# Performance work log

Measured on AMD Instinct MI355X. Metric: run time of the kernel, lower is better.

The kernel has to match this reference:

```python
import jax, jax.numpy as jnp
import numpy as np

N = 100000   # n_nodes
E = 1600000  # n_edges
BN_EPS = 1e-5


def setup_inputs() -> dict:
    key = jax.random.key(0)
    ks = jax.random.split(key, 10)
    x = jax.random.normal(ks[0], (N, 20), dtype=jnp.float32)
    edge_index = jax.random.randint(ks[1], (2, E), 0, N, dtype=jnp.int64)
    dims = [(20, 64), (64, 48), (48, 32)]
    inp = {"x": x, "edge_index": edge_index}
    for i, (di, do) in enumerate(dims):
        inp[f"W{i+1}"] = jax.random.normal(ks[2 + i], (di, do), dtype=jnp.float32) / np.sqrt(di)
        inp[f"b{i+1}"] = jnp.zeros((do,), dtype=jnp.float32)
        inp[f"g{i+1}"] = jnp.ones((do,), dtype=jnp.float32)
        inp[f"beta{i+1}"] = jnp.zeros((do,), dtype=jnp.float32)
    return inp


def _gcn_norm(edge_index):
    # add self loops, compute symmetric normalization D^-1/2 (A+I) D^-1/2
    loop = jnp.arange(N, dtype=edge_index.dtype)
    src = jnp.concatenate([edge_index[0], loop])
    dst = jnp.concatenate([edge_index[1], loop])
    deg = jax.ops.segment_sum(jnp.ones_like(src, dtype=jnp.float32), dst, num_segments=N)
    dinv = jax.lax.rsqrt(deg)  # deg >= 1 thanks to self loops
    norm = dinv[src] * dinv[dst]  # [E+N]
    return src, dst, norm


def _gcn_layer(h, src, dst, norm, W, b):
    m = h @ W                                  # [N, out]
    agg = jax.ops.segment_sum(m[src] * norm[:, None], dst, num_segments=N)
    return agg + b


def _batchnorm(x, g, beta):
    mu = jnp.mean(x, axis=0)
    var = jnp.mean(jnp.square(x - mu), axis=0)  # biased, as torch BN training
    return (x - mu) * jax.lax.rsqrt(var + BN_EPS) * g + beta


def reference(x, edge_index, W1, b1, g1, beta1, W2, b2, g2, beta2, W3, b3, g3, beta3):
    src, dst, norm = _gcn_norm(edge_index)
    h = _gcn_layer(x, src, dst, norm, W1, b1)
    h = jax.nn.relu(_batchnorm(h, g1, beta1))   # dropout rate 0 -> identity
    h = _gcn_layer(h, src, dst, norm, W2, b2)
    h = jax.nn.relu(_batchnorm(h, g2, beta2))
    h = _gcn_layer(h, src, dst, norm, W3, b3)
    h = _batchnorm(h, g3, beta3)                # last activation is Identity
    return h
```

## Files before the change

### kernel.cpp

```cpp
#include <hip/hip_runtime.h>


#define NN 100000
#define NE 1600000
constexpr float BN_EPS_F = 1e-5f;
constexpr float INVN = 1.f / (float)NN;

#define BSZ 128
#define NBKT ((NN + BSZ - 1) / BSZ)
#define EC 16384
#define NEB ((NE + EC - 1) / EC)
#define MTOT (NBKT * NEB)
#define CAP 4096


__device__ __forceinline__ unsigned f2bf(float f) {
  union { float f; unsigned u; } v; v.f = f;
  return (v.u + 0x7fffu + ((v.u >> 16) & 1u)) >> 16;
}
__device__ __forceinline__ unsigned pack_bf2(float f0, float f1) {
  return f2bf(f0) | (f2bf(f1) << 16);
}
__device__ __forceinline__ float bf_lo(unsigned u) {
  union { unsigned u; float f; } v; v.u = u << 16; return v.f;
}
__device__ __forceinline__ float bf_hi(unsigned u) {
  union { unsigned u; float f; } v; v.u = u & 0xffff0000u; return v.f;
}


__global__ void hist_pass(const int* __restrict__ dst, int* __restrict__ ph, int e) {
  __shared__ int h[NBKT];
  int tid = threadIdx.x;
  for (int i = tid; i < NBKT; i += 256) h[i] = 0;
  __syncthreads();
  int tbase = blockIdx.x * EC + tid * 64;
#pragma unroll 4
  for (int k = 0; k < 64; k += 4) {
    int i = tbase + k;
    if (i < e) {
      int4 d = *(const int4*)(dst + i);
      atomicAdd(&h[d.x >> 7], 1);
      atomicAdd(&h[d.y >> 7], 1);
      atomicAdd(&h[d.z >> 7], 1);
      atomicAdd(&h[d.w >> 7], 1);
    }
  }
  __syncthreads();
  for (int i = tid; i < NBKT; i += 256) ph[i * NEB + blockIdx.x] = h[i];
}

__global__ void scan_block_sums(const int* __restrict__ data, int* __restrict__ bsums, int n) {
  __shared__ int sd[256];
  int tid = threadIdx.x;
  int base = blockIdx.x * 1024;
  int s = 0;
#pragma unroll
  for (int j = 0; j < 4; j++) {
    int idx = base + tid * 4 + j;
    if (idx < n) s += data[idx];
  }
  sd[tid] = s;
  __syncthreads();
  for (int o = 128; o > 0; o >>= 1) {
    if (tid < o) sd[tid] += sd[tid + o];
    __syncthreads();
  }
  if (tid == 0) bsums[blockIdx.x] = sd[0];
}

__global__ void scan_bsums2(int* __restrict__ bsums, int nb) {
  __shared__ int sd[128];
  int tid = threadIdx.x;
  int v = (tid < nb) ? bsums[tid] : 0;
  sd[tid] = v;
  __syncthreads();
  for (int o = 1; o < 128; o <<= 1) {
    int t = (tid >= o) ? sd[tid - o] : 0;
    __syncthreads();
    sd[tid] += t;
    __syncthreads();
  }
  if (tid < nb) bsums[tid] = sd[tid] - v;
}

__global__ void scan_apply(int* __restrict__ data, const int* __restrict__ bsums, int n) {
  __shared__ int sd[256];
  int tid = threadIdx.x;
  int base = blockIdx.x * 1024;
  int c[4];
  int s = 0;
#pragma unroll
  for (int j = 0; j < 4; j++) {
    int idx = base + tid * 4 + j;
    c[j] = (idx < n) ? data[idx] : 0;
    s += c[j];
  }
  sd[tid] = s;
  __syncthreads();
  for (int o = 1; o < 256; o <<= 1) {
    int t = (tid >= o) ? sd[tid - o] : 0;
    __syncthreads();
    sd[tid] += t;
    __syncthreads();
  }
  int off = bsums[blockIdx.x] + sd[tid] - s;
#pragma unroll
  for (int j = 0; j < 4; j++) {
    int idx = base + tid * 4 + j;
    if (idx < n) {
      data[idx] = off;
      off += c[j];
    }
  }
}

__global__ void bin_pass(const int* __restrict__ src, const int* __restrict__ dst,
                         const int* __restrict__ ph, int* __restrict__ packed, int e) {
  __shared__ int cur[NBKT];
  int tid = threadIdx.x;
  for (int i = tid; i < NBKT; i += 256) cur[i] = ph[i * NEB + blockIdx.x];
  __syncthreads();
  int tbase = blockIdx.x * EC + tid * 64;
#pragma unroll 4
  for (int k = 0; k < 64; k += 4) {
    int i = tbase + k;
    if (i < e) {
      int4 s = *(const int4*)(src + i);
      int4 d = *(const int4*)(dst + i);
      int p0 = atomicAdd(&cur[d.x >> 7], 1);
      int p1 = atomicAdd(&cur[d.y >> 7], 1);
      int p2 = atomicAdd(&cur[d.z >> 7], 1);
      int p3 = atomicAdd(&cur[d.w >> 7], 1);
      packed[p0] = (s.x << 7) | (d.x & 127);
      packed[p1] = (s.y << 7) | (d.y & 127);
      packed[p2] = (s.z << 7) | (d.z & 127);
      packed[p3] = (s.w << 7) | (d.w & 127);
    }
  }
}

__global__ void bucket_finalize(const int* __restrict__ ph, const int* __restrict__ packed,
                                const float* __restrict__ x, int* __restrict__ rowptr,
                                float* __restrict__ dinv, int* __restrict__ csr_src,
                                unsigned* __restrict__ xb) {
  __shared__ int eidx[CAP];
  __shared__ int csr_l[CAP];
  __shared__ int ldeg[BSZ], lscan[BSZ], lcur[BSZ];
  __shared__ float ldinv[BSZ];
  int b = blockIdx.x, tid = threadIdx.x;
  int start = ph[b * NEB];
  int end = (b == NBKT - 1) ? NE : ph[(b + 1) * NEB];
  int cnt = end - start;
  if (cnt > CAP) cnt = CAP;
  for (int i = tid; i < cnt; i += 256) eidx[i] = packed[start + i];
  if (tid < BSZ) ldeg[tid] = 0;
  __syncthreads();
  for (int i = tid; i < cnt; i += 256) atomicAdd(&ldeg[eidx[i] & 127], 1);
  __syncthreads();
  if (tid < BSZ) lscan[tid] = ldeg[tid];
  __syncthreads();
  for (int o = 1; o < BSZ; o <<= 1) {
    int t = 0;
    if (tid < BSZ && tid >= o) t = lscan[tid - o];
    __syncthreads();
    if (tid < BSZ) lscan[tid] += t;
    __syncthreads();
  }
  int gn = b * BSZ + tid;
  if (tid < BSZ) {
    int ex = lscan[tid] - ldeg[tid];
    lcur[tid] = ex;
    float dv = rsqrtf((float)(ldeg[tid] + 1));
    ldinv[tid] = dv;
    if (gn < NN) {
      rowptr[gn] = start + ex;
      dinv[gn] = dv;
    }
  }
  if (b == NBKT - 1 && tid == 0) rowptr[NN] = NE;
  __syncthreads();
  for (int i = tid; i < cnt; i += 256) {
    int pe = eidx[i];
    int pos = atomicAdd(&lcur[pe & 127], 1);
    csr_l[pos] = pe >> 7;
  }
  __syncthreads();
  for (int i = tid; i < cnt; i += 256) csr_src[start + i] = csr_l[i];
  for (int i = tid; i < BSZ * 16; i += 256) {
    int nl = i >> 4, j = i & 15;
    int g2 = b * BSZ + nl;
    if (g2 < NN) {
      unsigned u = 0;
      if (j < 10) {
        float2 f = *(const float2*)(x + (size_t)g2 * 20 + 2 * j);
        float dd = ldinv[nl];
        u = pack_bf2(dd * f.x, dd * f.y);
      }
      xb[(size_t)g2 * 16 + j] = u;
    }
  }
}


__launch_bounds__(256)
__global__ void agg1_gemm1(const unsigned* __restrict__ mb, const int* __restrict__ rowptr,
                           const int* __restrict__ csr_src, const float* __restrict__ dinv,
                           const float* __restrict__ W1, const float* __restrict__ b1,
                           unsigned* __restrict__ h1u, float* __restrict__ gsum) {
  __shared__ float Wl[20 * 64];
  __shared__ float Hl[16][20];
  __shared__ float4 sbuf[256];
  int tid = threadIdx.x;
  for (int i = tid; i < 20 * 64; i += 256) Wl[i] = W1[i];
  int sub = tid >> 4, lane = tid & 15;
  int cl = (lane < 10) ? lane : lane - 10;
  int d = blockIdx.x * 16 + sub;
  int start = rowptr[d], end = rowptr[d + 1];
  unsigned su = mb[(size_t)d * 16 + cl];
  float acc0 = bf_lo(su), acc1 = bf_hi(su);
  int end1 = end - 1;
  for (int base = start; base < end; base += 16) {
    unsigned u[16];
#pragma unroll
    for (int t = 0; t < 16; t++) {
      int jt = base + t;
      int jc = jt < end1 ? jt : end1;
      unsigned uu = mb[(size_t)csr_src[jc] * 16 + cl];
      u[t] = (jt < end) ? uu : 0u;
    }
#pragma unroll
    for (int t = 0; t < 16; t++) { acc0 += bf_lo(u[t]); acc1 += bf_hi(u[t]); }
  }
  float dd = dinv[d];
  if (lane < 10) {
    Hl[sub][2 * cl] = dd * acc0;
    Hl[sub][2 * cl + 1] = dd * acc1;
  }
  __syncthreads();
  int cg = lane;
  float a0 = b1[4 * cg], a1 = b1[4 * cg + 1], a2 = b1[4 * cg + 2], a3 = b1[4 * cg + 3];
#pragma unroll
  for (int k = 0; k < 20; k++) {
    float a = Hl[sub][k];
    const float* w = &Wl[k * 64 + 4 * cg];
    a0 = fmaf(a, w[0], a0);
    a1 = fmaf(a, w[1], a1);
    a2 = fmaf(a, w[2], a2);
    a3 = fmaf(a, w[3], a3);
  }
  *(uint2*)(h1u + (size_t)d * 32 + 2 * cg) = make_uint2(pack_bf2(a0, a1), pack_bf2(a2, a3));
  sbuf[tid] = make_float4(a0, a1, a2, a3);
  __syncthreads();
  float* gs = gsum + (blockIdx.x & 7) * 128;
  if (tid < 16) {
    float s0 = 0.f, s1 = 0.f, s2 = 0.f, s3 = 0.f;
#pragma unroll
    for (int k = 0; k < 16; k++) {
      float4 a = sbuf[k * 16 + tid];
      s0 += a.x; s1 += a.y; s2 += a.z; s3 += a.w;
    }
    atomicAdd(&gs[4 * tid], s0);
    atomicAdd(&gs[4 * tid + 1], s1);
    atomicAdd(&gs[4 * tid + 2], s2);
    atomicAdd(&gs[4 * tid + 3], s3);
  }
  __syncthreads();
  sbuf[tid] = make_float4(a0 * a0, a1 * a1, a2 * a2, a3 * a3);
  __syncthreads();
  if (tid < 16) {
    float q0 = 0.f, q1 = 0.f, q2 = 0.f, q3 = 0.f;
#pragma unroll
    for (int k = 0; k < 16; k++) {
      float4 b = sbuf[k * 16 + tid];
      q0 += b.x; q1 += b.y; q2 += b.z; q3 += b.w;
    }
    atomicAdd(&gs[64 + 4 * tid], q0);
    atomicAdd(&gs[64 + 4 * tid + 1], q1);
    atomicAdd(&gs[64 + 4 * tid + 2], q2);
    atomicAdd(&gs[64 + 4 * tid + 3], q3);
  }
}


__launch_bounds__(256)
__global__ void gemm2_bf(const unsigned* __restrict__ hu, const float* __restrict__ W,
                         const float* __restrict__ gsum, const float* __restrict__ g,
                         const float* __restrict__ beta, const float* __restrict__ dinv,
                         unsigned* __restrict__ out) {
  __shared__ float Wl[64 * 48];
  __shared__ float Hl[16][64];
  __shared__ float scl[64], sft[64];
  int tid = threadIdx.x;
  int row0 = blockIdx.x * 16;
  if (tid < 64) {
    float s = 0.f, q = 0.f;
    for (int b = 0; b < 8; b++) {
      s += gsum[b * 128 + tid];
      q += gsum[b * 128 + 64 + tid];
    }
    float mean = s * INVN;
    float var = fmaxf(q * INVN - mean * mean, 0.f);
    float inv = rsqrtf(var + BN_EPS_F);
    float sc = g[tid] * inv;
    scl[tid] = sc;
    sft[tid] = beta[tid] - mean * sc;
  }
  for (int i = tid; i < 64 * 48; i += 256) Wl[i] = W[i];
  __syncthreads();
  for (int i = tid; i < 16 * 32; i += 256) {
    int r = i >> 5, j = i & 31;
    unsigned u = hu[(size_t)(row0 + r) * 32 + j];
    Hl[r][2 * j] = fmaxf(fmaf(bf_lo(u), scl[2 * j], sft[2 * j]), 0.f);
    Hl[r][2 * j + 1] = fmaxf(fmaf(bf_hi(u), scl[2 * j + 1], sft[2 * j + 1]), 0.f);
  }
  __syncthreads();
  int r = tid >> 4, c = tid & 15;
  if (c < 12) {
    float a0 = 0.f, a1 = 0.f, a2 = 0.f, a3 = 0.f;
#pragma unroll
    for (int k = 0; k < 64; k++) {
      float a = Hl[r][k];
      const float* w = &Wl[k * 48 + 4 * c];
      a0 = fmaf(a, w[0], a0);
      a1 = fmaf(a, w[1], a1);
      a2 = fmaf(a, w[2], a2);
      a3 = fmaf(a, w[3], a3);
    }
    float dd = dinv[row0 + r];
    uint2 uo = make_uint2(pack_bf2(dd * a0, dd * a1), pack_bf2(dd * a2, dd * a3));
    *(uint2*)(out + (size_t)(row0 + r) * 24 + 2 * c) = uo;
  }
}


__launch_bounds__(256)
__global__ void aggregate_bf48(const uint2* __restrict__ mb, const int* __restrict__ rowptr,
                               const int* __restrict__ csr_src, const float* __restrict__ dinv,
                               const float* __restrict__ bias, unsigned* __restrict__ out,
                               float* __restrict__ gsum) {
  __shared__ float4 sbuf[256];
  int tid = threadIdx.x;
  int sub = tid >> 4, lane = tid & 15;
  int cl = (lane < 12) ? lane : lane - 12;
  int d = blockIdx.x * 16 + sub;
  int start = rowptr[d], end = rowptr[d + 1];
  uint2 su = mb[(size_t)d * 12 + cl];
  float acc0 = bf_lo(su.x), acc1 = bf_hi(su.x), acc2 = bf_lo(su.y), acc3 = bf_hi(su.y);
  int end1 = end - 1;
  for (int base = start; base < end; base += 16) {
    uint2 u[16];
#pragma unroll
    for (int t = 0; t < 16; t++) {
      int jt = base + t;
      int jc = jt < end1 ? jt : end1;
      uint2 uu = mb[(size_t)csr_src[jc] * 12 + cl];
      u[t].x = (jt < end) ? uu.x : 0u;
      u[t].y = (jt < end) ? uu.y : 0u;
    }
#pragma unroll
    for (int t = 0; t < 16; t++) {
      acc0 += bf_lo(u[t].x); acc1 += bf_hi(u[t].x);
      acc2 += bf_lo(u[t].y); acc3 += bf_hi(u[t].y);
    }
  }
  float dd = dinv[d];
  float v0 = dd * acc0 + bias[4 * cl];
  float v1 = dd * acc1 + bias[4 * cl + 1];
  float v2 = dd * acc2 + bias[4 * cl + 2];
  float v3 = dd * acc3 + bias[4 * cl + 3];
  if (lane >= 12) { v0 = v1 = v2 = v3 = 0.f; }
  if (lane < 12) {
    uint2 uo = make_uint2(pack_bf2(v0, v1), pack_bf2(v2, v3));
    *(uint2*)(out + (size_t)d * 24 + 2 * cl) = uo;
  }
  sbuf[tid] = make_float4(v0, v1, v2, v3);
  __syncthreads();
  float* gs = gsum + (blockIdx.x & 7) * 128;
  if (tid < 12) {
    float s0 = 0.f, s1 = 0.f, s2 = 0.f, s3 = 0.f;
#pragma unroll
    for (int k = 0; k < 16; k++) {
      float4 a = sbuf[k * 16 + tid];
      s0 += a.x; s1 += a.y; s2 += a.z; s3 += a.w;
    }
    atomicAdd(&gs[4 * tid], s0);
    atomicAdd(&gs[4 * tid + 1], s1);
    atomicAdd(&gs[4 * tid + 2], s2);
    atomicAdd(&gs[4 * tid + 3], s3);
  }
  __syncthreads();
  sbuf[tid] = make_float4(v0 * v0, v1 * v1, v2 * v2, v3 * v3);
  __syncthreads();
  if (tid < 12) {
    float q0 = 0.f, q1 = 0.f, q2 = 0.f, q3 = 0.f;
#pragma unroll
    for (int k = 0; k < 16; k++) {
      float4 b = sbuf[k * 16 + tid];
      q0 += b.x; q1 += b.y; q2 += b.z; q3 += b.w;
    }
    atomicAdd(&gs[64 + 4 * tid], q0);
    atomicAdd(&gs[64 + 4 * tid + 1], q1);
    atomicAdd(&gs[64 + 4 * tid + 2], q2);
    atomicAdd(&gs[64 + 4 * tid + 3], q3);
  }
}


__launch_bounds__(256)
__global__ void gemm3_bf(const unsigned* __restrict__ hu, const float* __restrict__ W,
                         const float* __restrict__ gsum, const float* __restrict__ g,
                         const float* __restrict__ beta, const float* __restrict__ dinv,
                         unsigned* __restrict__ out) {
  __shared__ float Wl[48 * 32];
  __shared__ float Hl[16][48];
  __shared__ float scl[48], sft[48];
  int tid = threadIdx.x;
  int row0 = blockIdx.x * 16;
  if (tid < 48) {
    float s = 0.f, q = 0.f;
    for (int b = 0; b < 8; b++) {
      s += gsum[b * 128 + tid];
      q += gsum[b * 128 + 64 + tid];
    }
    float mean = s * INVN;
    float var = fmaxf(q * INVN - mean * mean, 0.f);
    float inv = rsqrtf(var + BN_EPS_F);
    float sc = g[tid] * inv;
    scl[tid] = sc;
    sft[tid] = beta[tid] - mean * sc;
  }
  for (int i = tid; i < 48 * 32; i += 256) Wl[i] = W[i];
  __syncthreads();
  for (int i = tid; i < 16 * 24; i += 256) {
    int r = i / 24, j = i % 24;
    unsigned u = hu[(size_t)(row0 + r) * 24 + j];
    Hl[r][2 * j] = fmaxf(fmaf(bf_lo(u), scl[2 * j], sft[2 * j]), 0.f);
    Hl[r][2 * j + 1] = fmaxf(fmaf(bf_hi(u), scl[2 * j + 1], sft[2 * j + 1]), 0.f);
  }
  __syncthreads();
  int r = tid >> 4, c2 = tid & 15;
  float a0 = 0.f, a1 = 0.f;
#pragma unroll
  for (int k = 0; k < 48; k++) {
    float a = Hl[r][k];
    a0 = fmaf(a, Wl[k * 32 + 2 * c2], a0);
    a1 = fmaf(a, Wl[k * 32 + 2 * c2 + 1], a1);
  }
  float dd = dinv[row0 + r];
  out[(size_t)(row0 + r) * 16 + c2] = pack_bf2(dd * a0, dd * a1);
}


__launch_bounds__(256)
__global__ void aggregate_bf32(const unsigned* __restrict__ mb, const int* __restrict__ rowptr,
                               const int* __restrict__ csr_src, const float* __restrict__ dinv,
                               const float* __restrict__ bias, unsigned* __restrict__ out,
                               float* __restrict__ gsum) {
  __shared__ float2 ssum[256], ssq[256];
  int tid = threadIdx.x;
  int sub = tid >> 4, lane = tid & 15;
  int d = blockIdx.x * 16 + sub;
  int start = rowptr[d], end = rowptr[d + 1];
  unsigned su = mb[(size_t)d * 16 + lane];
  float acc0 = bf_lo(su), acc1 = bf_hi(su);
  int end1 = end - 1;
  for (int base = start; base < end; base += 16) {
    unsigned u[16];
#pragma unroll
    for (int t = 0; t < 16; t++) {
      int jt = base + t;
      int jc = jt < end1 ? jt : end1;
      unsigned uu = mb[(size_t)csr_src[jc] * 16 + lane];
      u[t] = (jt < end) ? uu : 0u;
    }
#pragma unroll
    for (int t = 0; t < 16; t++) { acc0 += bf_lo(u[t]); acc1 += bf_hi(u[t]); }
  }
  float dd = dinv[d];
  float v0 = dd * acc0 + bias[2 * lane];
  float v1 = dd * acc1 + bias[2 * lane + 1];
  out[(size_t)d * 16 + lane] = pack_bf2(v0, v1);
  ssum[tid] = make_float2(v0, v1);
  ssq[tid] = make_float2(v0 * v0, v1 * v1);
  __syncthreads();
  if (tid < 16) {
    float s0 = 0.f, s1 = 0.f, q0 = 0.f, q1 = 0.f;
#pragma unroll
    for (int k = 0; k < 16; k++) {
      float2 a = ssum[k * 16 + tid];
      float2 b = ssq[k * 16 + tid];
      s0 += a.x; s1 += a.y; q0 += b.x; q1 += b.y;
    }
    float* gs = gsum + (blockIdx.x & 7) * 128;
    atomicAdd(&gs[2 * tid], s0);
    atomicAdd(&gs[2 * tid + 1], s1);
    atomicAdd(&gs[64 + 2 * tid], q0);
    atomicAdd(&gs[64 + 2 * tid + 1], q1);
  }
}


__launch_bounds__(256)
__global__ void bn_apply_out(const unsigned* __restrict__ hu, const float* __restrict__ gsum,
                             const float* __restrict__ g, const float* __restrict__ beta,
                             float* __restrict__ out) {
  __shared__ float scl[32], sft[32];
  int tid = threadIdx.x;
  if (tid < 32) {
    float s = 0.f, q = 0.f;
    for (int b = 0; b < 8; b++) {
      s += gsum[b * 128 + tid];
      q += gsum[b * 128 + 64 + tid];
    }
    float mean = s * INVN;
    float var = fmaxf(q * INVN - mean * mean, 0.f);
    float inv = rsqrtf(var + BN_EPS_F);
    float sc = g[tid] * inv;
    scl[tid] = sc;
    sft[tid] = beta[tid] - mean * sc;
  }
  __syncthreads();
  int base = (blockIdx.x * 256 + tid) * 4;
  int node = base >> 5;
  int c0 = base & 31;
  uint2 u = *(const uint2*)(hu + (size_t)node * 16 + (c0 >> 1));
  float4 o;
  o.x = bf_lo(u.x) * scl[c0] + sft[c0];
  o.y = bf_hi(u.x) * scl[c0 + 1] + sft[c0 + 1];
  o.z = bf_lo(u.y) * scl[c0 + 2] + sft[c0 + 2];
  o.w = bf_hi(u.y) * scl[c0 + 3] + sft[c0 + 3];
  *(float4*)(out + base) = o;
}


extern "C" void kernel_launch(void* const* d_in, const int* in_sizes, int n_in,
                              void* d_out, int out_size, void* d_ws, size_t ws_size,
                              hipStream_t stream) {
  const float* x = (const float*)d_in[0];
  const int* ei = (const int*)d_in[1];
  const float* W1 = (const float*)d_in[2];
  const float* b1 = (const float*)d_in[3];
  const float* g1 = (const float*)d_in[4];
  const float* be1 = (const float*)d_in[5];
  const float* W2 = (const float*)d_in[6];
  const float* b2 = (const float*)d_in[7];
  const float* g2 = (const float*)d_in[8];
  const float* be2 = (const float*)d_in[9];
  const float* W3 = (const float*)d_in[10];
  const float* b3 = (const float*)d_in[11];
  const float* g3 = (const float*)d_in[12];
  const float* be3 = (const float*)d_in[13];
  float* out = (float*)d_out;

  const int* src = ei;
  const int* dst = ei + NE;

  char* ws = (char*)d_ws;
  size_t off = 0;
  auto alloc = [&](size_t bytes) -> void* {
    void* p = ws + off;
    off += bytes;
    off = (off + 255) & ~(size_t)255;
    return p;
  };
  int* ph = (int*)alloc((size_t)MTOT * 4);
  int* bsums = (int*)alloc(128 * 4);
  int* packed = (int*)alloc((size_t)NE * 4);
  int* rowptr = (int*)alloc((NN + 1) * 4);
  int* csr_src = (int*)alloc((size_t)NE * 4);
  float* dinv = (float*)alloc(NN * 4);
  float* gsum = (float*)alloc(3 * 8 * 128 * 4);
  unsigned* xb = (unsigned*)alloc((size_t)NN * 16 * 4);
  unsigned* h1u = (unsigned*)alloc((size_t)NN * 32 * 4);
  unsigned* m2b = (unsigned*)alloc((size_t)NN * 24 * 4);
  unsigned* h2u = (unsigned*)alloc((size_t)NN * 24 * 4);

  unsigned* m3b = xb;
  unsigned* h3u = h1u;

  hipMemsetAsync(gsum, 0, 3 * 8 * 128 * 4, stream);

  const int nscan = (MTOT + 1023) / 1024;
  hist_pass<<<NEB, 256, 0, stream>>>(dst, ph, NE);
  scan_block_sums<<<nscan, 256, 0, stream>>>(ph, bsums, MTOT);
  scan_bsums2<<<1, 128, 0, stream>>>(bsums, nscan);
  scan_apply<<<nscan, 256, 0, stream>>>(ph, bsums, MTOT);
  bin_pass<<<NEB, 256, 0, stream>>>(src, dst, ph, packed, NE);
  bucket_finalize<<<NBKT, 256, 0, stream>>>(ph, packed, x, rowptr, dinv, csr_src, xb);

  agg1_gemm1<<<NN / 16, 256, 0, stream>>>(xb, rowptr, csr_src, dinv, W1, b1, h1u, gsum);

  gemm2_bf<<<NN / 16, 256, 0, stream>>>(h1u, W2, gsum, g1, be1, dinv, m2b);
  aggregate_bf48<<<NN / 16, 256, 0, stream>>>((const uint2*)m2b, rowptr, csr_src, dinv, b2, h2u,
                                              gsum + 1024);

  gemm3_bf<<<NN / 16, 256, 0, stream>>>(h2u, W3, gsum + 1024, g2, be2, dinv, m3b);
  aggregate_bf32<<<NN / 16, 256, 0, stream>>>(m3b, rowptr, csr_src, dinv, b3, h3u, gsum + 2048);

  bn_apply_out<<<NN * 32 / 1024, 256, 0, stream>>>(h3u, gsum + 2048, g3, be3, out);
}
```

Before: 375.0 us.

## Shrink edge chunks for binning and vectorize CSR index loads in aggregations

Cuts the edge chunk per block in the histogram and binning passes from 16384 to 4096 edges, so those passes launch about four times as many blocks. The prefix scan is widened to 4096 elements per block so the larger per-block histogram matrix still fits in one second-level scan. The three aggregation kernels now peel a few edges to reach 4-element alignment, then load CSR source indices as int4 vectors in full groups of 16, with a masked tail for the rest. The aim is better GPU occupancy during edge binning and fewer scalar index loads and clamps in the gather loops. The cost is a larger histogram and prefix array, plus more code paths.

```diff
diff --git a/kernel.cpp b/kernel.cpp
--- a/kernel.cpp
+++ b/kernel.cpp
@@ -8,10 +8,11 @@
 
 #define BSZ 128
 #define NBKT ((NN + BSZ - 1) / BSZ)
-#define EC 16384
+#define EC 4096
 #define NEB ((NE + EC - 1) / EC)
 #define MTOT (NBKT * NEB)
 #define CAP 4096
+#define SCH 4096
 
 
 __device__ __forceinline__ unsigned f2bf(float f) {
@@ -34,9 +35,9 @@
   int tid = threadIdx.x;
   for (int i = tid; i < NBKT; i += 256) h[i] = 0;
   __syncthreads();
-  int tbase = blockIdx.x * EC + tid * 64;
-#pragma unroll 4
-  for (int k = 0; k < 64; k += 4) {
+  int tbase = blockIdx.x * EC + tid * 16;
+#pragma unroll
+  for (int k = 0; k < 16; k += 4) {
     int i = tbase + k;
     if (i < e) {
       int4 d = *(const int4*)(dst + i);
@@ -53,11 +54,11 @@
 __global__ void scan_block_sums(const int* __restrict__ data, int* __restrict__ bsums, int n) {
   __shared__ int sd[256];
   int tid = threadIdx.x;
-  int base = blockIdx.x * 1024;
+  int base = blockIdx.x * SCH + tid * 16;
   int s = 0;
 #pragma unroll
-  for (int j = 0; j < 4; j++) {
-    int idx = base + tid * 4 + j;
+  for (int j = 0; j < 16; j++) {
+    int idx = base + j;
     if (idx < n) s += data[idx];
   }
   sd[tid] = s;
@@ -87,12 +88,12 @@
 __global__ void scan_apply(int* __restrict__ data, const int* __restrict__ bsums, int n) {
   __shared__ int sd[256];
   int tid = threadIdx.x;
-  int base = blockIdx.x * 1024;
-  int c[4];
+  int base = blockIdx.x * SCH + tid * 16;
+  int c[16];
   int s = 0;
 #pragma unroll
-  for (int j = 0; j < 4; j++) {
-    int idx = base + tid * 4 + j;
+  for (int j = 0; j < 16; j++) {
+    int idx = base + j;
     c[j] = (idx < n) ? data[idx] : 0;
     s += c[j];
   }
@@ -106,8 +107,8 @@
   }
   int off = bsums[blockIdx.x] + sd[tid] - s;
 #pragma unroll
-  for (int j = 0; j < 4; j++) {
-    int idx = base + tid * 4 + j;
+  for (int j = 0; j < 16; j++) {
+    int idx = base + j;
     if (idx < n) {
       data[idx] = off;
       off += c[j];
@@ -121,9 +122,9 @@
   int tid = threadIdx.x;
   for (int i = tid; i < NBKT; i += 256) cur[i] = ph[i * NEB + blockIdx.x];
   __syncthreads();
-  int tbase = blockIdx.x * EC + tid * 64;
-#pragma unroll 4
-  for (int k = 0; k < 64; k += 4) {
+  int tbase = blockIdx.x * EC + tid * 16;
+#pragma unroll
+  for (int k = 0; k < 16; k += 4) {
     int i = tbase + k;
     if (i < e) {
       int4 s = *(const int4*)(src + i);
@@ -219,13 +220,33 @@
   int start = rowptr[d], end = rowptr[d + 1];
   unsigned su = mb[(size_t)d * 16 + cl];
   float acc0 = bf_lo(su), acc1 = bf_hi(su);
-  int end1 = end - 1;
-  for (int base = start; base < end; base += 16) {
+  int j = start;
+  int aligned = (start + 3) & ~3;
+  int pe = aligned < end ? aligned : end;
+  for (; j < pe; j++) {
+    unsigned u = mb[(size_t)csr_src[j] * 16 + cl];
+    acc0 += bf_lo(u); acc1 += bf_hi(u);
+  }
+  for (; j + 16 <= end; j += 16) {
+    int4 s0 = *(const int4*)(csr_src + j);
+    int4 s1 = *(const int4*)(csr_src + j + 4);
+    int4 s2 = *(const int4*)(csr_src + j + 8);
+    int4 s3 = *(const int4*)(csr_src + j + 12);
+    int idx[16] = {s0.x, s0.y, s0.z, s0.w, s1.x, s1.y, s1.z, s1.w,
+                   s2.x, s2.y, s2.z, s2.w, s3.x, s3.y, s3.z, s3.w};
     unsigned u[16];
 #pragma unroll
+    for (int t = 0; t < 16; t++) u[t] = mb[(size_t)idx[t] * 16 + cl];
+#pragma unroll
+    for (int t = 0; t < 16; t++) { acc0 += bf_lo(u[t]); acc1 += bf_hi(u[t]); }
+  }
+  if (j < end) {
+    int e1 = end - 1;
+    unsigned u[16];
+#pragma unroll
     for (int t = 0; t < 16; t++) {
-      int jt = base + t;
-      int jc = jt < end1 ? jt : end1;
+      int jt = j + t;
+      int jc = jt < e1 ? jt : e1;
       unsigned uu = mb[(size_t)csr_src[jc] * 16 + cl];
       u[t] = (jt < end) ? uu : 0u;
     }
@@ -347,13 +368,36 @@
   int start = rowptr[d], end = rowptr[d + 1];
   uint2 su = mb[(size_t)d * 12 + cl];
   float acc0 = bf_lo(su.x), acc1 = bf_hi(su.x), acc2 = bf_lo(su.y), acc3 = bf_hi(su.y);
-  int end1 = end - 1;
-  for (int base = start; base < end; base += 16) {
+  int j = start;
+  int aligned = (start + 3) & ~3;
+  int pe = aligned < end ? aligned : end;
+  for (; j < pe; j++) {
+    uint2 u = mb[(size_t)csr_src[j] * 12 + cl];
+    acc0 += bf_lo(u.x); acc1 += bf_hi(u.x); acc2 += bf_lo(u.y); acc3 += bf_hi(u.y);
+  }
+  for (; j + 16 <= end; j += 16) {
+    int4 s0 = *(const int4*)(csr_src + j);
+    int4 s1 = *(const int4*)(csr_src + j + 4);
+    int4 s2 = *(const int4*)(csr_src + j + 8);
+    int4 s3 = *(const int4*)(csr_src + j + 12);
+    int idx[16] = {s0.x, s0.y, s0.z, s0.w, s1.x, s1.y, s1.z, s1.w,
+                   s2.x, s2.y, s2.z, s2.w, s3.x, s3.y, s3.z, s3.w};
     uint2 u[16];
 #pragma unroll
+    for (int t = 0; t < 16; t++) u[t] = mb[(size_t)idx[t] * 12 + cl];
+#pragma unroll
     for (int t = 0; t < 16; t++) {
-      int jt = base + t;
-      int jc = jt < end1 ? jt : end1;
+      acc0 += bf_lo(u[t].x); acc1 += bf_hi(u[t].x);
+      acc2 += bf_lo(u[t].y); acc3 += bf_hi(u[t].y);
+    }
+  }
+  if (j < end) {
+    int e1 = end - 1;
+    uint2 u[16];
+#pragma unroll
+    for (int t = 0; t < 16; t++) {
+      int jt = j + t;
+      int jc = jt < e1 ? jt : e1;
       uint2 uu = mb[(size_t)csr_src[jc] * 12 + cl];
       u[t].x = (jt < end) ? uu.x : 0u;
       u[t].y = (jt < end) ? uu.y : 0u;
@@ -464,13 +508,33 @@
   int start = rowptr[d], end = rowptr[d + 1];
   unsigned su = mb[(size_t)d * 16 + lane];
   float acc0 = bf_lo(su), acc1 = bf_hi(su);
-  int end1 = end - 1;
-  for (int base = start; base < end; base += 16) {
+  int j = start;
+  int aligned = (start + 3) & ~3;
+  int pe = aligned < end ? aligned : end;
+  for (; j < pe; j++) {
+    unsigned u = mb[(size_t)csr_src[j] * 16 + lane];
+    acc0 += bf_lo(u); acc1 += bf_hi(u);
+  }
+  for (; j + 16 <= end; j += 16) {
+    int4 s0 = *(const int4*)(csr_src + j);
+    int4 s1 = *(const int4*)(csr_src + j + 4);
+    int4 s2 = *(const int4*)(csr_src + j + 8);
+    int4 s3 = *(const int4*)(csr_src + j + 12);
+    int idx[16] = {s0.x, s0.y, s0.z, s0.w, s1.x, s1.y, s1.z, s1.w,
+                   s2.x, s2.y, s2.z, s2.w, s3.x, s3.y, s3.z, s3.w};
     unsigned u[16];
 #pragma unroll
+    for (int t = 0; t < 16; t++) u[t] = mb[(size_t)idx[t] * 16 + lane];
+#pragma unroll
+    for (int t = 0; t < 16; t++) { acc0 += bf_lo(u[t]); acc1 += bf_hi(u[t]); }
+  }
+  if (j < end) {
+    int e1 = end - 1;
+    unsigned u[16];
+#pragma unroll
     for (int t = 0; t < 16; t++) {
-      int jt = base + t;
-      int jc = jt < end1 ? jt : end1;
+      int jt = j + t;
+      int jc = jt < e1 ? jt : e1;
       unsigned uu = mb[(size_t)csr_src[jc] * 16 + lane];
       u[t] = (jt < end) ? uu : 0u;
     }
@@ -581,7 +645,7 @@
 
   hipMemsetAsync(gsum, 0, 3 * 8 * 128 * 4, stream);
 
-  const int nscan = (MTOT + 1023) / 1024;
+  const int nscan = (MTOT + SCH - 1) / SCH;
   hist_pass<<<NEB, 256, 0, stream>>>(dst, ph, NE);
   scan_block_sums<<<nscan, 256, 0, stream>>>(ph, bsums, MTOT);
   scan_bsums2<<<1, 128, 0, stream>>>(bsums, nscan);
```

Result: no change. 378.6 us (+1.0%).
